# Optimization experiments

Hardware: AMD Instinct MI355X
Metric: run time of the kernel (lower is better)

Reference implementation:

```python
import jax, jax.numpy as jnp
import numpy as np

DIM = 2048
N_HEADS = 16
HEAD_DIM = DIM // N_HEADS
GROUP_SIZE = 128
THRESHOLD = 0.5
EPS = 1e-8
B, T = 2, 2048


def _ternary_dequant(w):
    # groupwise absmean ternary quantize + dequant; DIM % GROUP_SIZE == 0 so no pad
    O, I = w.shape
    g = I // GROUP_SIZE
    wg = w.reshape(O, g, GROUP_SIZE)
    scale = jnp.clip(jnp.mean(jnp.abs(wg), axis=-1, keepdims=True), EPS)
    wn = wg / scale
    q = jnp.where(wn > THRESHOLD, 1.0, jnp.where(wn < -THRESHOLD, -1.0, 0.0))
    return (q * scale).reshape(O, I)


def _bitlinear(x, w):
    # STE: forward uses quantized weight
    w_ste = w + jax.lax.stop_gradient(_ternary_dequant(w) - w)
    return x @ w_ste.T


def _rope_tables(t, head_dim, base=10000.0):
    half = head_dim // 2
    inv_freq = 1.0 / (base ** (jnp.arange(half, dtype=jnp.float32) / half))
    freqs = jnp.outer(jnp.arange(t, dtype=jnp.float32), inv_freq)  # [T, half]
    return jnp.cos(freqs), jnp.sin(freqs)


def _apply_rope(x, cos, sin):
    # x: [B, H, T, D]
    d = x.shape[-1]
    x1, x2 = x[..., : d // 2], x[..., d // 2 :]
    cos = cos[None, None, :, :]
    sin = sin[None, None, :, :]
    return jnp.concatenate([x1 * cos - x2 * sin, x1 * sin + x2 * cos], axis=-1)


def setup_inputs() -> dict:
    key = jax.random.key(0)
    ks = jax.random.split(key, 5)
    std = 1.0 / np.sqrt(DIM)
    return {
        "x": jax.random.normal(ks[0], (B, T, DIM), dtype=jnp.float32),
        "w_q": jax.random.normal(ks[1], (DIM, DIM), dtype=jnp.float32) * std,
        "w_k": jax.random.normal(ks[2], (DIM, DIM), dtype=jnp.float32) * std,
        "w_v": jax.random.normal(ks[3], (DIM, DIM), dtype=jnp.float32) * std,
        "w_o": jax.random.normal(ks[4], (DIM, DIM), dtype=jnp.float32) * std,
    }


def reference(x, w_q, w_k, w_v, w_o):
    b, t, c = x.shape
    scale = HEAD_DIM ** -0.5

    def split_heads(y):
        return y.reshape(b, t, N_HEADS, HEAD_DIM).transpose(0, 2, 1, 3)  # [B,H,T,D]

    q = split_heads(_bitlinear(x, w_q))
    k = split_heads(_bitlinear(x, w_k))
    v = split_heads(_bitlinear(x, w_v))

    cos, sin = _rope_tables(t, HEAD_DIM)
    q = _apply_rope(q, cos, sin)
    k = _apply_rope(k, cos, sin)

    scores = jnp.einsum("bhqd,bhkd->bhqk", q, k) * scale
    causal = jnp.triu(jnp.ones((t, t), dtype=bool), k=1)
    scores = jnp.where(causal[None, None], -jnp.inf, scores)
    probs = jax.nn.softmax(scores, axis=-1)
    y = jnp.einsum("bhqk,bhkd->bhqd", probs, v)
    y = y.transpose(0, 2, 1, 3).reshape(b, t, c)
    return _bitlinear(y, w_o)
```

## Files before the change

### kernel.cpp

```cpp
#include <hip/hip_runtime.h>
#include <stdint.h>
#include <math.h>

#define DIMC 2048
#define NHEADS 16
#define HDIM 128
#define TSEQ 2048
#define NTOK 4096

using bf16x8 = __attribute__((ext_vector_type(8))) short;
using f32x4  = __attribute__((ext_vector_type(4))) float;

typedef __attribute__((address_space(1))) const void gas_void;
typedef __attribute__((address_space(3))) void las_void;

static __device__ __forceinline__ unsigned short f2b(float f) {
  union { float f; unsigned int u; } a; a.f = f;
  unsigned int u = a.u;
  u = (u + 0x7fffu + ((u >> 16) & 1u)) >> 16;
  return (unsigned short)u;
}
static __device__ __forceinline__ float b2f(unsigned short s) {
  union { unsigned int u; float f; } a; a.u = ((unsigned int)s) << 16;
  return a.f;
}

static __device__ __forceinline__ int detect_inline(const void* __restrict__ x)
{
  const int lane = threadIdx.x & 63;
  const unsigned short u = ((const unsigned short*)x)[2 * lane];
  const int e = (u >> 7) & 0xFF;
  const unsigned long long m = __ballot((e >= 112) && (e <= 135));
  return (__popcll(m) >= 32) ? 1 : 0;
}

static __device__ __forceinline__ void dequant_one(
    const void* __restrict__ w, unsigned short* __restrict__ o,
    int grp, int lane, int isbf16)
{
  float a, bq;
  if (isbf16) {
    const unsigned int pk =
        ((const unsigned int*)((const unsigned short*)w + (long)grp * 128))[lane];
    a  = b2f((unsigned short)(pk & 0xffffu));
    bq = b2f((unsigned short)(pk >> 16));
  } else {
    const float2 v = ((const float2*)((const float*)w + (long)grp * 128))[lane];
    a = v.x; bq = v.y;
  }
  double s = fabs((double)a) + fabs((double)bq);
  #pragma unroll
  for (int off = 1; off < 64; off <<= 1) s += __shfl_xor(s, off);
  double scale = s * (1.0 / 128.0);
  if (scale < 1e-8) scale = 1e-8;
  const float fs = (float)scale;
  const double wn0 = (double)a / scale;
  const double wn1 = (double)bq / scale;
  const float q0 = (wn0 > 0.5) ? fs : ((wn0 < -0.5) ? -fs : 0.0f);
  const float q1 = (wn1 > 0.5) ? fs : ((wn1 < -0.5) ? -fs : 0.0f);
  const unsigned int opk = (unsigned int)f2b(q0) | ((unsigned int)f2b(q1) << 16);
  ((unsigned int*)o)[(long)grp * 64 + lane] = opk;
}

__global__ void __launch_bounds__(256) prep(
    const void* __restrict__ x,
    const void* __restrict__ w0, const void* __restrict__ w1,
    const void* __restrict__ w2, const void* __restrict__ w3,
    unsigned short* __restrict__ xb, unsigned short* __restrict__ wqkv,
    unsigned short* __restrict__ wob)
{
  const int isbf16 = detect_inline(x);
  const int wave = threadIdx.x >> 6, lane = threadIdx.x & 63;
  const int y = blockIdx.y;
  if (y == 0) {
    const int i = (blockIdx.x * 256 + threadIdx.x) * 4;
    if (isbf16) {
      *(ushort4*)(xb + i) = *(const ushort4*)((const unsigned short*)x + i);
    } else {
      const float4 v = *(const float4*)((const float*)x + i);
      ushort4 u;
      u.x = f2b(v.x); u.y = f2b(v.y); u.z = f2b(v.z); u.w = f2b(v.w);
      *(ushort4*)(xb + i) = u;
    }
  } else if (y <= 3) {
    const void* w = (y == 1) ? w0 : (y == 2) ? w1 : w2;
    dequant_one(w, wqkv + (long)(y - 1) * DIMC * DIMC,
                blockIdx.x * 4 + wave, lane, isbf16);
  } else {
    dequant_one(w3, wob, blockIdx.x * 4 + wave, lane, isbf16);
  }
}

__global__ void __launch_bounds__(256) dequant_auto(
    const void* __restrict__ w, const void* __restrict__ x,
    unsigned short* __restrict__ o)
{
  const int isbf16 = detect_inline(x);
  dequant_one(w, o, blockIdx.x * 4 + (threadIdx.x >> 6), threadIdx.x & 63,
              isbf16);
}

static __device__ __forceinline__ void gemm8_core(
    const unsigned short* __restrict__ A, const unsigned short* __restrict__ Bm,
    int m0, int n0, int K, f32x4 (&acc)[4][4],
    unsigned short (*sm)[3][8192])
{
  const int tid = threadIdx.x;
  const int w = tid >> 6, lane = tid & 63;
  const int wr = w >> 1, wc = w & 1;
  const int c16 = lane & 15, q4 = lane >> 4;
  const int swz = (c16 * 32 + q4 * 8) ^ ((c16 & 8) ? 16 : 0);
  const int srow = lane >> 2;
  const int scol = ((lane & 3) * 8) ^ ((lane & 32) ? 16 : 0);
  const int rg0 = w >> 1, cg = w & 1;
  const int NT = K >> 6;

  #pragma unroll
  for (int i = 0; i < 4; i++)
    #pragma unroll
    for (int j = 0; j < 4; j++) acc[i][j] = (f32x4){0.f, 0.f, 0.f, 0.f};

  auto stage = [&](const unsigned short* __restrict__ G, int rowbase, int kt,
                   unsigned short* dst) {
    #pragma unroll
    for (int l = 0; l < 2; l++) {
      const unsigned short* s = G +
          (long)(rowbase + (rg0 + l * 4) * 16 + srow) * K + kt * 64 + cg * 32 + scol;
      __builtin_amdgcn_global_load_lds((gas_void*)s,
          (las_void*)(dst + (l * 8 + w) * 512), 16, 0, 0);
    }
  };

  stage(A,  m0,       0, sm[0][0]);
  stage(A,  m0 + 128, 0, sm[0][1]);
  stage(Bm, n0,       0, sm[0][2]);
  stage(Bm, n0,       1, sm[1][2]);
  asm volatile("s_waitcnt vmcnt(2)" ::: "memory");
  __builtin_amdgcn_s_barrier();

  bf16x8 af[4][2], b01[2][2], b23[2][2];
  const int ah = wr >> 1;
  const int abase = (wr & 1) * 4096;
  const int bbase = wc * 4096;

  for (int t = 0; t < NT; ++t) {
    const int cur = t & 1, nxt = cur ^ 1;

    #pragma unroll
    for (int m = 0; m < 4; m++)
      #pragma unroll
      for (int kk = 0; kk < 2; kk++)
        af[m][kk] = *(const bf16x8*)&sm[cur][ah][abase + m * 1024 + kk * 512 + swz];
    #pragma unroll
    for (int n = 0; n < 2; n++)
      #pragma unroll
      for (int kk = 0; kk < 2; kk++) {
        b01[n][kk] = *(const bf16x8*)&sm[cur][2][bbase + n * 1024 + kk * 512 + swz];
        b23[n][kk] = *(const bf16x8*)&sm[cur][2][bbase + (2 + n) * 1024 + kk * 512 + swz];
      }
    if (t + 1 < NT) {
      stage(A, m0,       t + 1, sm[nxt][0]);
      stage(A, m0 + 128, t + 1, sm[nxt][1]);
    }
    __builtin_amdgcn_s_barrier();
    asm volatile("s_waitcnt lgkmcnt(0)" ::: "memory");
    __builtin_amdgcn_s_setprio(1);
    #pragma unroll
    for (int kk = 0; kk < 2; kk++)
      #pragma unroll
      for (int m = 0; m < 4; m++)
        #pragma unroll
        for (int n = 0; n < 2; n++)
          acc[m][n] = __builtin_amdgcn_mfma_f32_16x16x32_bf16(
              af[m][kk], b01[n][kk], acc[m][n], 0, 0, 0);
    __builtin_amdgcn_s_setprio(0);
    __builtin_amdgcn_s_barrier();

    if (t + 2 < NT) stage(Bm, n0, t + 2, sm[cur][2]);
    __builtin_amdgcn_s_setprio(1);
    #pragma unroll
    for (int kk = 0; kk < 2; kk++)
      #pragma unroll
      for (int m = 0; m < 4; m++)
        #pragma unroll
        for (int n = 0; n < 2; n++)
          acc[m][2 + n] = __builtin_amdgcn_mfma_f32_16x16x32_bf16(
              af[m][kk], b23[n][kk], acc[m][2 + n], 0, 0, 0);
    __builtin_amdgcn_s_setprio(0);
    if (t + 1 < NT) {
      if (t + 2 < NT) { asm volatile("s_waitcnt vmcnt(2)" ::: "memory"); }
      else            { asm volatile("s_waitcnt vmcnt(0)" ::: "memory"); }
      __builtin_amdgcn_s_barrier();
    }
  }
}

__global__ void __launch_bounds__(512, 2) gemm8_qkv(
    const unsigned short* __restrict__ A, const unsigned short* __restrict__ Bm,
    unsigned short* __restrict__ C0, unsigned short* __restrict__ C1,
    unsigned short* __restrict__ C2, int K)
{
  __shared__ unsigned short sm[2][3][8192];
  const int n0 = blockIdx.x * 128;
  const int m0 = blockIdx.y * 256;
  f32x4 acc[4][4];
  gemm8_core(A, Bm, m0, n0, K, acc, sm);

  unsigned short* Cb = (n0 < 2048) ? C0 : (n0 < 4096) ? C1 : C2;
  const int w = threadIdx.x >> 6, lane = threadIdx.x & 63;
  const int wr = w >> 1, wc = w & 1;
  const int c16 = lane & 15, q4 = lane >> 4;
  const int nloc = (n0 & 2047) + wc * 64;
  #pragma unroll
  for (int mt = 0; mt < 4; mt++) {
    const int m = m0 + wr * 64 + mt * 16 + q4 * 4;
    #pragma unroll
    for (int nt = 0; nt < 4; nt++) {
      const int n = nloc + nt * 16 + c16;
      #pragma unroll
      for (int r = 0; r < 4; r++)
        Cb[(long)(m + r) * DIMC + n] = f2b(acc[mt][nt][r]);
    }
  }
}

__global__ void __launch_bounds__(512, 2) gemm8_bt(
    const unsigned short* __restrict__ A, const unsigned short* __restrict__ Bm,
    float* __restrict__ C, int N, int K)
{
  __shared__ unsigned short sm[2][3][8192];
  const int n0 = blockIdx.x * 128;
  const int m0 = blockIdx.y * 256;
  f32x4 acc[4][4];
  gemm8_core(A, Bm, m0, n0, K, acc, sm);

  const int w = threadIdx.x >> 6, lane = threadIdx.x & 63;
  const int wr = w >> 1, wc = w & 1;
  const int c16 = lane & 15, q4 = lane >> 4;
  #pragma unroll
  for (int mt = 0; mt < 4; mt++) {
    const int m = m0 + wr * 64 + mt * 16 + q4 * 4;
    #pragma unroll
    for (int nt = 0; nt < 4; nt++) {
      const int n = n0 + wc * 64 + nt * 16 + c16;
      #pragma unroll
      for (int r = 0; r < 4; r++)
        C[(long)(m + r) * N + n] = acc[mt][nt][r];
    }
  }
}

__global__ void __launch_bounds__(256) rope_kernel(
    unsigned short* __restrict__ Q, unsigned short* __restrict__ Kb)
{
  const int idx = blockIdx.x * 256 + threadIdx.x;
  const int d4 = (idx & 15) * 4;
  const int h = (idx >> 4) & (NHEADS - 1);
  const int row = idx >> 8;
  const int t = row & (TSEQ - 1);
  const long base = (long)row * DIMC + h * HDIM + d4;

  ushort4 q1 = *(ushort4*)(Q + base), q2 = *(ushort4*)(Q + base + 64);
  ushort4 k1 = *(ushort4*)(Kb + base), k2 = *(ushort4*)(Kb + base + 64);
  unsigned short* q1p = (unsigned short*)&q1;
  unsigned short* q2p = (unsigned short*)&q2;
  unsigned short* k1p = (unsigned short*)&k1;
  unsigned short* k2p = (unsigned short*)&k2;

  #pragma unroll
  for (int j = 0; j < 4; j++) {
    const int d = d4 + j;
    const float inv_freq = expf(-9.210340371976184f * (float)d * (1.0f / 64.0f));
    float sn, cs;
    sincosf((float)t * inv_freq, &sn, &cs);
    float x1 = b2f(q1p[j]), x2 = b2f(q2p[j]);
    q1p[j] = f2b(x1 * cs - x2 * sn);
    q2p[j] = f2b(x1 * sn + x2 * cs);
    x1 = b2f(k1p[j]); x2 = b2f(k2p[j]);
    k1p[j] = f2b(x1 * cs - x2 * sn);
    k2p[j] = f2b(x1 * sn + x2 * cs);
  }
  *(ushort4*)(Q + base) = q1;  *(ushort4*)(Q + base + 64) = q2;
  *(ushort4*)(Kb + base) = k1; *(ushort4*)(Kb + base + 64) = k2;
}

#define FA_M 16.0f
__global__ void __launch_bounds__(256) fattn(
    const unsigned short* __restrict__ Q,
    const unsigned short* __restrict__ K,
    const unsigned short* __restrict__ V,
    unsigned short* __restrict__ Y)
{
  __shared__ unsigned short SU[9216];
  __shared__ unsigned short VT[128 * 72];
  __shared__ float red[4][32];

  const int tid = threadIdx.x, wave = tid >> 6, lane = tid & 63;
  const int idx = blockIdx.x;
  const int qt = 15 - (idx >> 5);
  const int bh = idx & 31;
  const int b = bh >> 4, h = bh & 15;
  const int qbase = qt * 128;
  const int qw = wave * 32;
  const int c = lane & 15, g = lane >> 4;
  const long tokbase = (long)b * TSEQ;
  const int col0 = h * HDIM;

  bf16x8 qf[2][4];
  #pragma unroll
  for (int qq = 0; qq < 2; qq++) {
    const unsigned short* qp =
        Q + (tokbase + qbase + qw + qq * 16 + c) * DIMC + col0 + g * 8;
    #pragma unroll
    for (int kc = 0; kc < 4; kc++) qf[qq][kc] = *(const bf16x8*)(qp + kc * 32);
  }

  f32x4 od[8][2];
  #pragma unroll
  for (int dt = 0; dt < 8; dt++)
    #pragma unroll
    for (int qq = 0; qq < 2; qq++)
      od[dt][qq] = (f32x4){0.f, 0.f, 0.f, 0.f};
  float lpart[2][4];
  #pragma unroll
  for (int qq = 0; qq < 2; qq++)
    #pragma unroll
    for (int r = 0; r < 4; r++) lpart[qq][r] = 0.0f;

  const int ksr = tid >> 2, ksc = (tid & 3) * 32;
  const int vk0 = (tid & 31) * 2, vd0 = (tid >> 5) * 16;

  const float SC = 0.088388347648318447f;
  const int nkt = 2 * qt + 2;

  float4 kr0, kr1, kr2, kr3;
  bf16x8 va0, va1, vb0, vb1;
  {
    const unsigned short* src = K + (tokbase + ksr) * DIMC + col0 + ksc;
    kr0 = ((const float4*)src)[0]; kr1 = ((const float4*)src)[1];
    kr2 = ((const float4*)src)[2]; kr3 = ((const float4*)src)[3];
    const unsigned short* s0 = V + (tokbase + vk0) * DIMC + col0 + vd0;
    const unsigned short* s1 = s0 + DIMC;
    va0 = *(const bf16x8*)(s0); va1 = *(const bf16x8*)(s0 + 8);
    vb0 = *(const bf16x8*)(s1); vb1 = *(const bf16x8*)(s1 + 8);
  }

  for (int kt = 0; kt < nkt; kt++) {
    const int kb = kt * 64;
    __syncthreads();
    {
      float4* dst = (float4*)&SU[ksr * 136 + ksc];
      dst[0] = kr0; dst[1] = kr1; dst[2] = kr2; dst[3] = kr3;
    }
    {
      #pragma unroll
      for (int dd = 0; dd < 8; dd++) {
        const unsigned int p0 =
            (unsigned int)(unsigned short)va0[dd] |
            ((unsigned int)(unsigned short)vb0[dd] << 16);
        *(unsigned int*)&VT[(vd0 + dd) * 72 + vk0] = p0;
      }
      #pragma unroll
      for (int dd = 0; dd < 8; dd++) {
        const unsigned int p1 =
            (unsigned int)(unsigned short)va1[dd] |
            ((unsigned int)(unsigned short)vb1[dd] << 16);
        *(unsigned int*)&VT[(vd0 + 8 + dd) * 72 + vk0] = p1;
      }
    }
    __syncthreads();

    if (kt + 1 < nkt) {
      const int kb2 = kb + 64;
      const unsigned short* src = K + (tokbase + kb2 + ksr) * DIMC + col0 + ksc;
      kr0 = ((const float4*)src)[0]; kr1 = ((const float4*)src)[1];
      kr2 = ((const float4*)src)[2]; kr3 = ((const float4*)src)[3];
      const unsigned short* s0 = V + (tokbase + kb2 + vk0) * DIMC + col0 + vd0;
      const unsigned short* s1 = s0 + DIMC;
      va0 = *(const bf16x8*)(s0); va1 = *(const bf16x8*)(s0 + 8);
      vb0 = *(const bf16x8*)(s1); vb1 = *(const bf16x8*)(s1 + 8);
    }

    f32x4 sacc[2][4];
    #pragma unroll
    for (int qq = 0; qq < 2; qq++)
      #pragma unroll
      for (int nt = 0; nt < 4; nt++) sacc[qq][nt] = (f32x4){0.f, 0.f, 0.f, 0.f};
    #pragma unroll
    for (int kc = 0; kc < 4; kc++) {
      bf16x8 bk[4];
      #pragma unroll
      for (int nt = 0; nt < 4; nt++)
        bk[nt] = *(const bf16x8*)&SU[(nt * 16 + c) * 136 + kc * 32 + g * 8];
      #pragma unroll
      for (int qq = 0; qq < 2; qq++)
        #pragma unroll
        for (int nt = 0; nt < 4; nt++)
          sacc[qq][nt] = __builtin_amdgcn_mfma_f32_16x16x32_bf16(
              qf[qq][kc], bk[nt], sacc[qq][nt], 0, 0, 0);
    }
    __syncthreads();

    #pragma unroll
    for (int qq = 0; qq < 2; qq++)
      #pragma unroll
      for (int r = 0; r < 4; r++) {
        const int qg = qbase + qw + qq * 16 + g * 4 + r;
        #pragma unroll
        for (int nt = 0; nt < 4; nt++) {
          const int kg = kb + nt * 16 + c;
          const float sv = sacc[qq][nt][r] * SC - FA_M;
          const float p = (kg > qg) ? 0.0f : __expf(sv);
          lpart[qq][r] += p;
          SU[(wave * 32 + qq * 16 + g * 4 + r) * 72 + nt * 16 + c] = f2b(p);
        }
      }

    #pragma unroll
    for (int kc = 0; kc < 2; kc++) {
      bf16x8 pb[2];
      #pragma unroll
      for (int qq = 0; qq < 2; qq++)
        pb[qq] = *(const bf16x8*)&SU[(wave * 32 + qq * 16 + c) * 72 + kc * 32 + g * 8];
      #pragma unroll
      for (int dt = 0; dt < 8; dt++) {
        bf16x8 va = *(const bf16x8*)&VT[(dt * 16 + c) * 72 + kc * 32 + g * 8];
        #pragma unroll
        for (int qq = 0; qq < 2; qq++)
          od[dt][qq] = __builtin_amdgcn_mfma_f32_16x16x32_bf16(
              va, pb[qq], od[dt][qq], 0, 0, 0);
      }
    }
  }

  #pragma unroll
  for (int qq = 0; qq < 2; qq++)
    #pragma unroll
    for (int r = 0; r < 4; r++) {
      float l = lpart[qq][r];
      #pragma unroll
      for (int off = 1; off < 16; off <<= 1) l += __shfl_xor(l, off);
      lpart[qq][r] = l;
    }
  __syncthreads();
  if (c == 0) {
    #pragma unroll
    for (int qq = 0; qq < 2; qq++)
      #pragma unroll
      for (int r = 0; r < 4; r++)
        red[wave][qq * 16 + g * 4 + r] = 1.0f / lpart[qq][r];
  }
  __syncthreads();
  #pragma unroll
  for (int qq = 0; qq < 2; qq++) {
    const float linv = red[wave][qq * 16 + c];
    unsigned short* yp =
        Y + (tokbase + qbase + qw + qq * 16 + c) * DIMC + col0;
    #pragma unroll
    for (int dt = 0; dt < 8; dt++)
      #pragma unroll
      for (int r = 0; r < 4; r++)
        yp[dt * 16 + g * 4 + r] = f2b(od[dt][qq][r] * linv);
  }
}

extern "C" void kernel_launch(void* const* d_in, const int* in_sizes, int n_in,
                              void* d_out, int out_size, void* d_ws, size_t ws_size,
                              hipStream_t stream)
{
  const void* x  = d_in[0];
  const void* wq = d_in[1];
  const void* wk = d_in[2];
  const void* wv = d_in[3];
  const void* wo = d_in[4];
  float* out = (float*)d_out;

  char* ws = (char*)d_ws;
  const size_t MB = 1024 * 1024;
  unsigned short* wbuf = (unsigned short*)(ws + 0 * MB);
  unsigned short* xb   = (unsigned short*)(ws + 24 * MB);
  unsigned short* Qb   = (unsigned short*)(ws + 40 * MB);
  unsigned short* Kb   = (unsigned short*)(ws + 56 * MB);
  unsigned short* Vb   = (unsigned short*)(ws + 72 * MB);
  unsigned short* wob  = (unsigned short*)(ws + 88 * MB);
  unsigned short* Yb   = xb;

  const int wo_in_prep = (ws_size >= 97 * MB) ? 1 : 0;

  prep<<<dim3(8192, wo_in_prep ? 5 : 4), 256, 0, stream>>>(
      x, wq, wk, wv, wo, xb, wbuf, wob);
  gemm8_qkv<<<dim3(48, 16), 512, 0, stream>>>(xb, wbuf, Qb, Kb, Vb, DIMC);
  rope_kernel<<<dim3(4096), 256, 0, stream>>>(Qb, Kb);
  fattn<<<dim3(512), 256, 0, stream>>>(Qb, Kb, Vb, Yb);
  const unsigned short* wo_b;
  if (wo_in_prep) {
    wo_b = wob;
  } else {
    dequant_auto<<<dim3(8192), 256, 0, stream>>>(wo, x, wbuf);
    wo_b = wbuf;
  }
  gemm8_bt<<<dim3(16, 16), 512, 0, stream>>>(Yb, wo_b, out, DIMC, DIMC);
}
```

Before: 391.7 us.

## Fuse RoPE into QKV GEMM epilogue and swap grid mapping

Removes the separate rope_kernel and applies rotary embedding in the QKV GEMM epilogue. Each head's 128-wide tile is split across two waves, which exchange fp32 accumulators through shared memory so each can pair x1 with x2. This avoids a full read-modify-write pass over Q and K in global memory and one kernel launch. The grid is also transposed so consecutive blocks walk M, and the dequant threshold test now compares against 0.5*scale instead of dividing. In exchange the epilogue gains extra barriers and shared-memory traffic.

After: 428.9 us. 1.1x slower.

```diff
diff --git a/kernel.cpp b/kernel.cpp
--- a/kernel.cpp
+++ b/kernel.cpp
@@ -54,10 +54,10 @@
   double scale = s * (1.0 / 128.0);
   if (scale < 1e-8) scale = 1e-8;
   const float fs = (float)scale;
-  const double wn0 = (double)a / scale;
-  const double wn1 = (double)bq / scale;
-  const float q0 = (wn0 > 0.5) ? fs : ((wn0 < -0.5) ? -fs : 0.0f);
-  const float q1 = (wn1 > 0.5) ? fs : ((wn1 < -0.5) ? -fs : 0.0f);
+  const double hs = 0.5 * scale;
+  const double da = (double)a, db = (double)bq;
+  const float q0 = (da > hs) ? fs : ((da < -hs) ? -fs : 0.0f);
+  const float q1 = (db > hs) ? fs : ((db < -hs) ? -fs : 0.0f);
   const unsigned int opk = (unsigned int)f2b(q0) | ((unsigned int)f2b(q1) << 16);
   ((unsigned int*)o)[(long)grp * 64 + lane] = opk;
 }
@@ -201,8 +201,8 @@
     unsigned short* __restrict__ C2, int K)
 {
   __shared__ unsigned short sm[2][3][8192];
-  const int n0 = blockIdx.x * 128;
-  const int m0 = blockIdx.y * 256;
+  const int m0 = blockIdx.x * 256;
+  const int n0 = blockIdx.y * 128;
   f32x4 acc[4][4];
   gemm8_core(A, Bm, m0, n0, K, acc, sm);
 
@@ -211,15 +211,48 @@
   const int wr = w >> 1, wc = w & 1;
   const int c16 = lane & 15, q4 = lane >> 4;
   const int nloc = (n0 & 2047) + wc * 64;
-  #pragma unroll
-  for (int mt = 0; mt < 4; mt++) {
-    const int m = m0 + wr * 64 + mt * 16 + q4 * 4;
-    #pragma unroll
-    for (int nt = 0; nt < 4; nt++) {
-      const int n = nloc + nt * 16 + c16;
-      #pragma unroll
-      for (int r = 0; r < 4; r++)
-        Cb[(long)(m + r) * DIMC + n] = f2b(acc[mt][nt][r]);
+
+  if (n0 < 4096) {
+    float* stg = (float*)&sm[0][0][0];
+    const int pw = wr * 2 + (wc ^ 1);
+    __syncthreads();
+    for (int mt = 0; mt < 4; mt++) {
+      #pragma unroll
+      for (int nt = 0; nt < 4; nt++)
+        #pragma unroll
+        for (int r = 0; r < 4; r++)
+          stg[w * 1024 + (q4 * 4 + r) * 64 + nt * 16 + c16] = acc[mt][nt][r];
+      __syncthreads();
+      #pragma unroll
+      for (int nt = 0; nt < 4; nt++) {
+        const int d = nt * 16 + c16;
+        const float inv_freq =
+            expf(-9.210340371976184f * (float)d * (1.0f / 64.0f));
+        #pragma unroll
+        for (int r = 0; r < 4; r++) {
+          const int m = m0 + wr * 64 + mt * 16 + q4 * 4 + r;
+          float sn, cs;
+          sincosf((float)(m & (TSEQ - 1)) * inv_freq, &sn, &cs);
+          const float other = stg[pw * 1024 + (q4 * 4 + r) * 64 + d];
+          const float own = acc[mt][nt][r];
+          const float outv = (wc == 0) ? (own * cs - other * sn)
+                                       : (other * sn + own * cs);
+          Cb[(long)m * DIMC + nloc + d] = f2b(outv);
+        }
+      }
+      __syncthreads();
+    }
+  } else {
+    #pragma unroll
+    for (int mt = 0; mt < 4; mt++) {
+      const int m = m0 + wr * 64 + mt * 16 + q4 * 4;
+      #pragma unroll
+      for (int nt = 0; nt < 4; nt++) {
+        const int n = nloc + nt * 16 + c16;
+        #pragma unroll
+        for (int r = 0; r < 4; r++)
+          Cb[(long)(m + r) * DIMC + n] = f2b(acc[mt][nt][r]);
+      }
     }
   }
 }
@@ -248,40 +281,6 @@
         C[(long)(m + r) * N + n] = acc[mt][nt][r];
     }
   }
-}
-
-__global__ void __launch_bounds__(256) rope_kernel(
-    unsigned short* __restrict__ Q, unsigned short* __restrict__ Kb)
-{
-  const int idx = blockIdx.x * 256 + threadIdx.x;
-  const int d4 = (idx & 15) * 4;
-  const int h = (idx >> 4) & (NHEADS - 1);
-  const int row = idx >> 8;
-  const int t = row & (TSEQ - 1);
-  const long base = (long)row * DIMC + h * HDIM + d4;
-
-  ushort4 q1 = *(ushort4*)(Q + base), q2 = *(ushort4*)(Q + base + 64);
-  ushort4 k1 = *(ushort4*)(Kb + base), k2 = *(ushort4*)(Kb + base + 64);
-  unsigned short* q1p = (unsigned short*)&q1;
-  unsigned short* q2p = (unsigned short*)&q2;
-  unsigned short* k1p = (unsigned short*)&k1;
-  unsigned short* k2p = (unsigned short*)&k2;
-
-  #pragma unroll
-  for (int j = 0; j < 4; j++) {
-    const int d = d4 + j;
-    const float inv_freq = expf(-9.210340371976184f * (float)d * (1.0f / 64.0f));
-    float sn, cs;
-    sincosf((float)t * inv_freq, &sn, &cs);
-    float x1 = b2f(q1p[j]), x2 = b2f(q2p[j]);
-    q1p[j] = f2b(x1 * cs - x2 * sn);
-    q2p[j] = f2b(x1 * sn + x2 * cs);
-    x1 = b2f(k1p[j]); x2 = b2f(k2p[j]);
-    k1p[j] = f2b(x1 * cs - x2 * sn);
-    k2p[j] = f2b(x1 * sn + x2 * cs);
-  }
-  *(ushort4*)(Q + base) = q1;  *(ushort4*)(Q + base + 64) = q2;
-  *(ushort4*)(Kb + base) = k1; *(ushort4*)(Kb + base + 64) = k2;
 }
 
 #define FA_M 16.0f
@@ -489,8 +488,7 @@
 
   prep<<<dim3(8192, wo_in_prep ? 5 : 4), 256, 0, stream>>>(
       x, wq, wk, wv, wo, xb, wbuf, wob);
-  gemm8_qkv<<<dim3(48, 16), 512, 0, stream>>>(xb, wbuf, Qb, Kb, Vb, DIMC);
-  rope_kernel<<<dim3(4096), 256, 0, stream>>>(Qb, Kb);
+  gemm8_qkv<<<dim3(16, 48), 512, 0, stream>>>(xb, wbuf, Qb, Kb, Vb, DIMC);
   fattn<<<dim3(512), 256, 0, stream>>>(Qb, Kb, Vb, Yb);
   const unsigned short* wo_b;
   if (wo_in_prep) {
```

## Triple-buffer A tiles in GEMM core to prefetch two k-steps ahead

Applied to the files above, without the earlier changes.

The A operand tiles in the shared GEMM core move from double to triple buffering, so A loads are issued two k-iterations ahead instead of one. Wait counts are adjusted to match the extra in-flight loads. LDS use per block grows from 96KB to 128KB, which may cut how many blocks fit per CU alongside the 2-block launch bound. Separately, the dequant threshold test now compares against half the scale instead of dividing by the scale, removing double-precision divides in weight prep.

Measured after the change: 393.3 us. About the same (+0.4%).

```diff
diff --git a/kernel.cpp b/kernel.cpp
--- a/kernel.cpp
+++ b/kernel.cpp
@@ -54,10 +54,10 @@
   double scale = s * (1.0 / 128.0);
   if (scale < 1e-8) scale = 1e-8;
   const float fs = (float)scale;
-  const double wn0 = (double)a / scale;
-  const double wn1 = (double)bq / scale;
-  const float q0 = (wn0 > 0.5) ? fs : ((wn0 < -0.5) ? -fs : 0.0f);
-  const float q1 = (wn1 > 0.5) ? fs : ((wn1 < -0.5) ? -fs : 0.0f);
+  const double hs = 0.5 * scale;
+  const double da = (double)a, db = (double)bq;
+  const float q0 = (da > hs) ? fs : ((da < -hs) ? -fs : 0.0f);
+  const float q1 = (db > hs) ? fs : ((db < -hs) ? -fs : 0.0f);
   const unsigned int opk = (unsigned int)f2b(q0) | ((unsigned int)f2b(q1) << 16);
   ((unsigned int*)o)[(long)grp * 64 + lane] = opk;
 }
@@ -103,7 +103,7 @@
 static __device__ __forceinline__ void gemm8_core(
     const unsigned short* __restrict__ A, const unsigned short* __restrict__ Bm,
     int m0, int n0, int K, f32x4 (&acc)[4][4],
-    unsigned short (*sm)[3][8192])
+    unsigned short (*smA)[2][8192], unsigned short (*smB)[8192])
 {
   const int tid = threadIdx.x;
   const int w = tid >> 6, lane = tid & 63;
@@ -131,11 +131,13 @@
     }
   };
 
-  stage(A,  m0,       0, sm[0][0]);
-  stage(A,  m0 + 128, 0, sm[0][1]);
-  stage(Bm, n0,       0, sm[0][2]);
-  stage(Bm, n0,       1, sm[1][2]);
-  asm volatile("s_waitcnt vmcnt(2)" ::: "memory");
+  stage(A,  m0,       0, smA[0][0]);
+  stage(A,  m0 + 128, 0, smA[0][1]);
+  stage(Bm, n0,       0, smB[0]);
+  stage(A,  m0,       1, smA[1][0]);
+  stage(A,  m0 + 128, 1, smA[1][1]);
+  stage(Bm, n0,       1, smB[1]);
+  asm volatile("s_waitcnt vmcnt(6)" ::: "memory");
   __builtin_amdgcn_s_barrier();
 
   bf16x8 af[4][2], b01[2][2], b23[2][2];
@@ -143,24 +145,25 @@
   const int abase = (wr & 1) * 4096;
   const int bbase = wc * 4096;
 
+  int ai = 0, a2 = 2;
   for (int t = 0; t < NT; ++t) {
-    const int cur = t & 1, nxt = cur ^ 1;
+    const int bi = t & 1;
 
     #pragma unroll
     for (int m = 0; m < 4; m++)
       #pragma unroll
       for (int kk = 0; kk < 2; kk++)
-        af[m][kk] = *(const bf16x8*)&sm[cur][ah][abase + m * 1024 + kk * 512 + swz];
+        af[m][kk] = *(const bf16x8*)&smA[ai][ah][abase + m * 1024 + kk * 512 + swz];
     #pragma unroll
     for (int n = 0; n < 2; n++)
       #pragma unroll
       for (int kk = 0; kk < 2; kk++) {
-        b01[n][kk] = *(const bf16x8*)&sm[cur][2][bbase + n * 1024 + kk * 512 + swz];
-        b23[n][kk] = *(const bf16x8*)&sm[cur][2][bbase + (2 + n) * 1024 + kk * 512 + swz];
+        b01[n][kk] = *(const bf16x8*)&smB[bi][bbase + n * 1024 + kk * 512 + swz];
+        b23[n][kk] = *(const bf16x8*)&smB[bi][bbase + (2 + n) * 1024 + kk * 512 + swz];
       }
-    if (t + 1 < NT) {
-      stage(A, m0,       t + 1, sm[nxt][0]);
-      stage(A, m0 + 128, t + 1, sm[nxt][1]);
+    if (t + 2 < NT) {
+      stage(A, m0,       t + 2, smA[a2][0]);
+      stage(A, m0 + 128, t + 2, smA[a2][1]);
     }
     __builtin_amdgcn_s_barrier();
     asm volatile("s_waitcnt lgkmcnt(0)" ::: "memory");
@@ -176,7 +179,7 @@
     __builtin_amdgcn_s_setprio(0);
     __builtin_amdgcn_s_barrier();
 
-    if (t + 2 < NT) stage(Bm, n0, t + 2, sm[cur][2]);
+    if (t + 2 < NT) stage(Bm, n0, t + 2, smB[bi]);
     __builtin_amdgcn_s_setprio(1);
     #pragma unroll
     for (int kk = 0; kk < 2; kk++)
@@ -188,10 +191,12 @@
               af[m][kk], b23[n][kk], acc[m][2 + n], 0, 0, 0);
     __builtin_amdgcn_s_setprio(0);
     if (t + 1 < NT) {
-      if (t + 2 < NT) { asm volatile("s_waitcnt vmcnt(2)" ::: "memory"); }
+      if (t + 2 < NT) { asm volatile("s_waitcnt vmcnt(6)" ::: "memory"); }
       else            { asm volatile("s_waitcnt vmcnt(0)" ::: "memory"); }
       __builtin_amdgcn_s_barrier();
     }
+    ai = (ai == 2) ? 0 : ai + 1;
+    a2 = (a2 == 2) ? 0 : a2 + 1;
   }
 }
 
@@ -200,11 +205,12 @@
     unsigned short* __restrict__ C0, unsigned short* __restrict__ C1,
     unsigned short* __restrict__ C2, int K)
 {
-  __shared__ unsigned short sm[2][3][8192];
+  __shared__ unsigned short smA[3][2][8192];
+  __shared__ unsigned short smB[2][8192];
   const int n0 = blockIdx.x * 128;
   const int m0 = blockIdx.y * 256;
   f32x4 acc[4][4];
-  gemm8_core(A, Bm, m0, n0, K, acc, sm);
+  gemm8_core(A, Bm, m0, n0, K, acc, smA, smB);
 
   unsigned short* Cb = (n0 < 2048) ? C0 : (n0 < 4096) ? C1 : C2;
   const int w = threadIdx.x >> 6, lane = threadIdx.x & 63;
@@ -228,11 +234,12 @@
     const unsigned short* __restrict__ A, const unsigned short* __restrict__ Bm,
     float* __restrict__ C, int N, int K)
 {
-  __shared__ unsigned short sm[2][3][8192];
+  __shared__ unsigned short smA[3][2][8192];
+  __shared__ unsigned short smB[2][8192];
   const int n0 = blockIdx.x * 128;
   const int m0 = blockIdx.y * 256;
   f32x4 acc[4][4];
-  gemm8_core(A, Bm, m0, n0, K, acc, sm);
+  gemm8_core(A, Bm, m0, n0, K, acc, smA, smB);
 
   const int w = threadIdx.x >> 6, lane = threadIdx.x & 63;
   const int wr = w >> 1, wc = w & 1;
```
